# Kernel optimization log

Measured on AMD Instinct MI355X. Metric: run time of the kernel, lower is better.

## Reference

```python
import jax, jax.numpy as jnp
import numpy as np

N_NODES = 50000
N_EDGES = 800000
IN_DIM = 512
OUT_DIM = 512


def setup_inputs() -> dict:
    key = jax.random.key(0)
    ks = jax.random.split(key, 8)
    x = jax.random.normal(ks[0], (N_NODES, IN_DIM), dtype=jnp.float32)
    edge_index = jax.random.randint(ks[1], (2, N_EDGES), 0, N_NODES, dtype=jnp.int64)
    s = 1.0 / np.sqrt(IN_DIM)
    # SAGEConv params: lin_l (applied to aggregated neighbors, with bias),
    # lin_r (applied to root/self features, no bias). Two convs: loc and scale.
    Wl1 = jax.random.uniform(ks[2], (OUT_DIM, IN_DIM), jnp.float32, -s, s)
    bl1 = jnp.zeros((OUT_DIM,), jnp.float32)
    Wr1 = jax.random.uniform(ks[3], (OUT_DIM, IN_DIM), jnp.float32, -s, s)
    Wl2 = jax.random.uniform(ks[4], (OUT_DIM, IN_DIM), jnp.float32, -s, s)
    bl2 = jnp.zeros((OUT_DIM,), jnp.float32)
    Wr2 = jax.random.uniform(ks[5], (OUT_DIM, IN_DIM), jnp.float32, -s, s)
    return {"x": x, "edge_index": edge_index,
            "Wl1": Wl1, "bl1": bl1, "Wr1": Wr1,
            "Wl2": Wl2, "bl2": bl2, "Wr2": Wr2}


def _sage_conv(x, agg, Wl, bl, Wr):
    # lin_l(sum-aggregated neighbors) + lin_r(x)
    return agg @ Wl.T + bl + x @ Wr.T


def reference(x, edge_index, Wl1, bl1, Wr1, Wl2, bl2, Wr2):
    src, dst = edge_index[0], edge_index[1]
    # sum aggregation of source features into destination nodes: [N, in_dim]
    agg = jax.ops.segment_sum(x[src], dst, num_segments=N_NODES)
    loc = _sage_conv(x, agg, Wl1, bl1, Wr1)
    loc = jnp.clip(loc, -100.0, 100.0)
    scale = jax.nn.softplus(_sage_conv(x, agg, Wl2, bl2, Wr2)) + 0.001
    scale = jnp.minimum(scale, 100.0)
    return (loc, scale)
```

## Files before the change

### kernel.cpp

```cpp
#include <hip/hip_runtime.h>
#include <stdint.h>

#define N_NODES 50000
#define N_EDGES 800000
#define IN_DIM 512
#define OUT_DIM 512
#define KDIM 1024
#define NDIM 1024

typedef __bf16 bf16x8 __attribute__((ext_vector_type(8)));
typedef float f32x4 __attribute__((ext_vector_type(4)));

__device__ __forceinline__ unsigned short f2bf(float f) {
    union { float f; unsigned u; } c; c.f = f;
    unsigned u = c.u;
    u += 0x7fffu + ((u >> 16) & 1u);
    return (unsigned short)(u >> 16);
}
__device__ __forceinline__ float bf2f(unsigned short h) {
    union { unsigned u; float f; } c; c.u = ((unsigned)h) << 16;
    return c.f;
}

__global__ void xconv_kernel(const float* __restrict__ x, unsigned short* __restrict__ xb) {
    int i = blockIdx.x * blockDim.x + threadIdx.x;
    const int n4 = N_NODES * IN_DIM / 4;
    if (i < n4) {
        float4 v = ((const float4*)x)[i];
        ushort4 o;
        o.x = f2bf(v.x); o.y = f2bf(v.y); o.z = f2bf(v.z); o.w = f2bf(v.w);
        ((ushort4*)xb)[i] = o;
    }
}

__global__ void count_kernel(const int* __restrict__ ei, int* __restrict__ counts) {
    int i = blockIdx.x * blockDim.x + threadIdx.x;
    if (i < N_EDGES) {
        int dst = ei[N_EDGES + i];
        dst = min(max(dst, 0), N_NODES - 1);
        atomicAdd(&counts[dst], 1);
    }
}

__global__ __launch_bounds__(1024) void scan_local_kernel(
    const int* __restrict__ cnt, int* __restrict__ offs,
    int* __restrict__ bsums, int n) {
    __shared__ int warp_sums[16];
    int tid = threadIdx.x;
    int lane = tid & 63;
    int w = tid >> 6;
    int i = blockIdx.x * 1024 + tid;
    int v = (i < n) ? cnt[i] : 0;
    int s = v;
    #pragma unroll
    for (int d = 1; d < 64; d <<= 1) {
        int t = __shfl_up(s, d, 64);
        if (lane >= d) s += t;
    }
    if (lane == 63) warp_sums[w] = s;
    __syncthreads();
    if (w == 0) {
        int ws = (lane < 16) ? warp_sums[lane] : 0;
        #pragma unroll
        for (int d = 1; d < 16; d <<= 1) {
            int t = __shfl_up(ws, d, 64);
            if (lane >= d) ws += t;
        }
        if (lane < 16) warp_sums[lane] = ws;
    }
    __syncthreads();
    int base = (w > 0 ? warp_sums[w - 1] : 0);
    if (i < n) offs[i] = base + s - v;
    if (tid == 1023) bsums[blockIdx.x] = base + s;
}

__global__ void scan_bsums_kernel(int* __restrict__ bsums, int nb) {
    int lane = threadIdx.x & 63;
    int v = (lane < nb) ? bsums[lane] : 0;
    int s = v;
    #pragma unroll
    for (int d = 1; d < 64; d <<= 1) {
        int t = __shfl_up(s, d, 64);
        if (lane >= d) s += t;
    }
    if (lane < nb) bsums[lane] = s - v;
}

__global__ __launch_bounds__(1024) void scan_apply_kernel(
    int* __restrict__ offs, int* __restrict__ cursor,
    const int* __restrict__ bsums, const int* __restrict__ cnt, int n) {
    int i = blockIdx.x * 1024 + threadIdx.x;
    if (i < n) {
        int o = offs[i] + bsums[blockIdx.x];
        offs[i] = o;
        cursor[i] = o;
        if (i == n - 1) offs[n] = o + cnt[i];
    }
}

__global__ void fill_kernel(const int* __restrict__ ei, int* __restrict__ cursor,
                            int* __restrict__ bucket) {
    int i = blockIdx.x * blockDim.x + threadIdx.x;
    if (i < N_EDGES) {
        int src = ei[i];
        int dst = ei[N_EDGES + i];
        src = min(max(src, 0), N_NODES - 1);
        dst = min(max(dst, 0), N_NODES - 1);
        int pos = atomicAdd(&cursor[dst], 1);
        bucket[pos] = src;
    }
}

__global__ __launch_bounds__(256) void aggregate_kernel(
    const unsigned short* __restrict__ xb, const int* __restrict__ offs,
    const int* __restrict__ bucket, unsigned short* __restrict__ aggb) {
    int wid = threadIdx.x >> 6;
    int lane = threadIdx.x & 63;
    int n = blockIdx.x * 4 + wid;
    if (n >= N_NODES) return;
    int beg = offs[n], end = offs[n + 1];
    float a0[8] = {}, a1[8] = {};
    int e = beg;
    for (; e + 4 <= end; e += 4) {
        int s0 = bucket[e + 0];
        int s1 = bucket[e + 1];
        int s2 = bucket[e + 2];
        int s3 = bucket[e + 3];
        uint4 v0 = *(const uint4*)(xb + (size_t)s0 * IN_DIM + lane * 8);
        uint4 v1 = *(const uint4*)(xb + (size_t)s1 * IN_DIM + lane * 8);
        uint4 v2 = *(const uint4*)(xb + (size_t)s2 * IN_DIM + lane * 8);
        uint4 v3 = *(const uint4*)(xb + (size_t)s3 * IN_DIM + lane * 8);
        a0[0] += bf2f((unsigned short)(v0.x & 0xffffu)); a0[1] += bf2f((unsigned short)(v0.x >> 16));
        a0[2] += bf2f((unsigned short)(v0.y & 0xffffu)); a0[3] += bf2f((unsigned short)(v0.y >> 16));
        a0[4] += bf2f((unsigned short)(v0.z & 0xffffu)); a0[5] += bf2f((unsigned short)(v0.z >> 16));
        a0[6] += bf2f((unsigned short)(v0.w & 0xffffu)); a0[7] += bf2f((unsigned short)(v0.w >> 16));
        a1[0] += bf2f((unsigned short)(v1.x & 0xffffu)); a1[1] += bf2f((unsigned short)(v1.x >> 16));
        a1[2] += bf2f((unsigned short)(v1.y & 0xffffu)); a1[3] += bf2f((unsigned short)(v1.y >> 16));
        a1[4] += bf2f((unsigned short)(v1.z & 0xffffu)); a1[5] += bf2f((unsigned short)(v1.z >> 16));
        a1[6] += bf2f((unsigned short)(v1.w & 0xffffu)); a1[7] += bf2f((unsigned short)(v1.w >> 16));
        a0[0] += bf2f((unsigned short)(v2.x & 0xffffu)); a0[1] += bf2f((unsigned short)(v2.x >> 16));
        a0[2] += bf2f((unsigned short)(v2.y & 0xffffu)); a0[3] += bf2f((unsigned short)(v2.y >> 16));
        a0[4] += bf2f((unsigned short)(v2.z & 0xffffu)); a0[5] += bf2f((unsigned short)(v2.z >> 16));
        a0[6] += bf2f((unsigned short)(v2.w & 0xffffu)); a0[7] += bf2f((unsigned short)(v2.w >> 16));
        a1[0] += bf2f((unsigned short)(v3.x & 0xffffu)); a1[1] += bf2f((unsigned short)(v3.x >> 16));
        a1[2] += bf2f((unsigned short)(v3.y & 0xffffu)); a1[3] += bf2f((unsigned short)(v3.y >> 16));
        a1[4] += bf2f((unsigned short)(v3.z & 0xffffu)); a1[5] += bf2f((unsigned short)(v3.z >> 16));
        a1[6] += bf2f((unsigned short)(v3.w & 0xffffu)); a1[7] += bf2f((unsigned short)(v3.w >> 16));
    }
    for (; e < end; ++e) {
        int s = bucket[e];
        uint4 v = *(const uint4*)(xb + (size_t)s * IN_DIM + lane * 8);
        a0[0] += bf2f((unsigned short)(v.x & 0xffffu)); a0[1] += bf2f((unsigned short)(v.x >> 16));
        a0[2] += bf2f((unsigned short)(v.y & 0xffffu)); a0[3] += bf2f((unsigned short)(v.y >> 16));
        a0[4] += bf2f((unsigned short)(v.z & 0xffffu)); a0[5] += bf2f((unsigned short)(v.z >> 16));
        a0[6] += bf2f((unsigned short)(v.w & 0xffffu)); a0[7] += bf2f((unsigned short)(v.w >> 16));
    }
    uint4 o;
    o.x = (unsigned)f2bf(a0[0] + a1[0]) | ((unsigned)f2bf(a0[1] + a1[1]) << 16);
    o.y = (unsigned)f2bf(a0[2] + a1[2]) | ((unsigned)f2bf(a0[3] + a1[3]) << 16);
    o.z = (unsigned)f2bf(a0[4] + a1[4]) | ((unsigned)f2bf(a0[5] + a1[5]) << 16);
    o.w = (unsigned)f2bf(a0[6] + a1[6]) | ((unsigned)f2bf(a0[7] + a1[7]) << 16);
    *(uint4*)(aggb + (size_t)n * IN_DIM + lane * 8) = o;
}

__global__ void wconv_kernel(const float* __restrict__ Wl1, const float* __restrict__ Wr1,
                             const float* __restrict__ Wl2, const float* __restrict__ Wr2,
                             unsigned short* __restrict__ Wb) {
    int i = blockIdx.x * blockDim.x + threadIdx.x;
    if (i < NDIM * KDIM) {
        int n = i >> 10, k = i & 1023;
        const float* src;
        if (n < 512) src = (k < 512) ? Wl1 : Wr1;
        else         src = (k < 512) ? Wl2 : Wr2;
        int nn = n & 511, kk = k & 511;
        Wb[i] = f2bf(src[nn * 512 + kk]);
    }
}

#define BM 128
#define BN 128
#define BK 64
#define NT_TILES (NDIM / BN)
#define MT_TILES ((N_NODES + BM - 1) / BM)
#define NWG (NT_TILES * MT_TILES)

__device__ __forceinline__ void async_copy16(const void* g, void* lds) {
    __builtin_amdgcn_global_load_lds((const __attribute__((address_space(1))) void*)g,
                                     (__attribute__((address_space(3))) void*)lds, 16, 0, 0);
}

__global__ __launch_bounds__(256, 2) void gemm_kernel(
    const unsigned short* __restrict__ aggb,
    const unsigned short* __restrict__ xb,
    const unsigned short* __restrict__ Wb,
    const float* __restrict__ bl1, const float* __restrict__ bl2,
    float* __restrict__ out) {
    constexpr int M = N_NODES;
    __shared__ unsigned short sA[BM * BK];
    __shared__ unsigned short sB[BN * BK];

    int bid = blockIdx.x;
    int logical = (bid & 7) * (NWG / 8) + (bid >> 3);
    int nt = logical & (NT_TILES - 1);
    int mt = logical >> 3;
    int n0 = nt * BN;
    int m0 = mt * BM;

    int tid = threadIdx.x;
    int lane = tid & 63;
    int w = tid >> 6;
    int wm = (w >> 1) * 64, wn = (w & 1) * 64;

    f32x4 acc[4][4] = {};

    int fr = lane & 15, q = lane >> 4;
    int sl0 = ((q ^ (fr & 7)) << 3);
    int sl1 = (((q + 4) ^ (fr & 7)) << 3);

    for (int k0 = 0; k0 < KDIM; k0 += BK) {
        const unsigned short* Asrc;
        int ak;
        if (k0 < 512) { Asrc = aggb; ak = k0; } else { Asrc = xb; ak = k0 - 512; }
        #pragma unroll
        for (int iss = 0; iss < 4; ++iss) {
            int C = iss * 256 + tid;
            int r = C >> 3, p = C & 7;
            int gr = m0 + r; if (gr >= M) gr = M - 1;
            const unsigned short* g = Asrc + (size_t)gr * 512 + ak + ((p ^ (r & 7)) << 3);
            async_copy16(g, sA + (size_t)(iss * 256 + w * 64) * 8);
        }
        #pragma unroll
        for (int iss = 0; iss < 4; ++iss) {
            int C = iss * 256 + tid;
            int r = C >> 3, p = C & 7;
            const unsigned short* g = Wb + (size_t)(n0 + r) * KDIM + k0 + ((p ^ (r & 7)) << 3);
            async_copy16(g, sB + (size_t)(iss * 256 + w * 64) * 8);
        }
        __syncthreads();

        #pragma unroll
        for (int ksub = 0; ksub < 2; ++ksub) {
            int sl = ksub ? sl1 : sl0;
            bf16x8 af[4], bfg[4];
            #pragma unroll
            for (int i = 0; i < 4; ++i)
                af[i] = *(const bf16x8*)(sA + (wm + i * 16 + fr) * BK + sl);
            #pragma unroll
            for (int j = 0; j < 4; ++j)
                bfg[j] = *(const bf16x8*)(sB + (wn + j * 16 + fr) * BK + sl);
            #pragma unroll
            for (int i = 0; i < 4; ++i)
                #pragma unroll
                for (int j = 0; j < 4; ++j)
                    acc[i][j] = __builtin_amdgcn_mfma_f32_16x16x32_bf16(af[i], bfg[j], acc[i][j], 0, 0, 0);
        }
        __syncthreads();
    }

    bool is_scale = (n0 >= 512);
    const float* bias = is_scale ? bl2 : bl1;
    float* obase = out + (is_scale ? (size_t)N_NODES * OUT_DIM : 0);
    int ncol0 = is_scale ? (n0 - 512) : n0;
    int rq = lane >> 4;
    #pragma unroll
    for (int i = 0; i < 4; ++i) {
        #pragma unroll
        for (int j = 0; j < 4; ++j) {
            int colg = ncol0 + wn + j * 16 + fr;
            float b = bias[colg];
            #pragma unroll
            for (int r = 0; r < 4; ++r) {
                int rowg = m0 + wm + i * 16 + rq * 4 + r;
                if (rowg < M) {
                    float v = acc[i][j][r] + b;
                    float res;
                    if (is_scale) {
                        float sp = fmaxf(v, 0.f) + __logf(1.f + __expf(-fabsf(v)));
                        res = fminf(sp + 0.001f, 100.f);
                    } else {
                        res = fminf(fmaxf(v, -100.f), 100.f);
                    }
                    __builtin_nontemporal_store(res, &obase[(size_t)rowg * OUT_DIM + colg]);
                }
            }
        }
    }
}

extern "C" void kernel_launch(void* const* d_in, const int* in_sizes, int n_in,
                              void* d_out, int out_size, void* d_ws, size_t ws_size,
                              hipStream_t stream) {
    const float* x       = (const float*)d_in[0];
    const int* ei        = (const int*)d_in[1];
    const float* Wl1     = (const float*)d_in[2];
    const float* bl1     = (const float*)d_in[3];
    const float* Wr1     = (const float*)d_in[4];
    const float* Wl2     = (const float*)d_in[5];
    const float* bl2     = (const float*)d_in[6];
    const float* Wr2     = (const float*)d_in[7];
    float* out = (float*)d_out;

    char* ws = (char*)d_ws;
    size_t off = 0;
    auto alloc = [&](size_t bytes) -> void* {
        void* p = ws + off;
        off = (off + bytes + 255) & ~(size_t)255;
        return p;
    };
    unsigned short* xb    = (unsigned short*)alloc((size_t)N_NODES * IN_DIM * 2);
    unsigned short* aggb  = (unsigned short*)alloc((size_t)N_NODES * IN_DIM * 2);
    unsigned short* Wb    = (unsigned short*)alloc((size_t)NDIM * KDIM * 2);
    int* counts           = (int*)alloc((size_t)(N_NODES + 1) * 4);
    int* offs             = (int*)alloc((size_t)(N_NODES + 1) * 4);
    int* cursor           = (int*)alloc((size_t)N_NODES * 4);
    int* bucket           = (int*)alloc((size_t)N_EDGES * 4);
    int* bsums            = (int*)alloc(64 * 4);

    hipMemsetAsync(counts, 0, (size_t)(N_NODES + 1) * 4, stream);

    const int nb = (N_NODES + 1023) / 1024;

    xconv_kernel<<<(N_NODES * IN_DIM / 4 + 255) / 256, 256, 0, stream>>>(x, xb);
    count_kernel<<<(N_EDGES + 255) / 256, 256, 0, stream>>>(ei, counts);
    scan_local_kernel<<<nb, 1024, 0, stream>>>(counts, offs, bsums, N_NODES);
    scan_bsums_kernel<<<1, 64, 0, stream>>>(bsums, nb);
    scan_apply_kernel<<<nb, 1024, 0, stream>>>(offs, cursor, bsums, counts, N_NODES);
    fill_kernel<<<(N_EDGES + 255) / 256, 256, 0, stream>>>(ei, cursor, bucket);
    aggregate_kernel<<<(N_NODES + 3) / 4, 256, 0, stream>>>(xb, offs, bucket, aggb);
    wconv_kernel<<<(NDIM * KDIM + 255) / 256, 256, 0, stream>>>(Wl1, Wr1, Wl2, Wr2, Wb);

    gemm_kernel<<<NWG, 256, 0, stream>>>(aggb, xb, Wb, bl1, bl2, out);
}
```

Baseline: 600.0 us.

## Fuse prep kernels, merge scan steps, unroll gather, double-buffer GEMM LDS

```diff
diff --git a/kernel.cpp b/kernel.cpp
--- a/kernel.cpp
+++ b/kernel.cpp
@@ -22,23 +22,43 @@
     return c.f;
 }
 
-__global__ void xconv_kernel(const float* __restrict__ x, unsigned short* __restrict__ xb) {
-    int i = blockIdx.x * blockDim.x + threadIdx.x;
-    const int n4 = N_NODES * IN_DIM / 4;
-    if (i < n4) {
-        float4 v = ((const float4*)x)[i];
-        ushort4 o;
-        o.x = f2bf(v.x); o.y = f2bf(v.y); o.z = f2bf(v.z); o.w = f2bf(v.w);
-        ((ushort4*)xb)[i] = o;
-    }
-}
-
-__global__ void count_kernel(const int* __restrict__ ei, int* __restrict__ counts) {
-    int i = blockIdx.x * blockDim.x + threadIdx.x;
-    if (i < N_EDGES) {
-        int dst = ei[N_EDGES + i];
-        dst = min(max(dst, 0), N_NODES - 1);
-        atomicAdd(&counts[dst], 1);
+#define XCONV_BLOCKS ((N_NODES * IN_DIM / 4 + 255) / 256)
+#define COUNT_BLOCKS ((N_EDGES + 255) / 256)
+#define WCONV_BLOCKS ((NDIM * KDIM + 255) / 256)
+
+__global__ __launch_bounds__(256) void prep_kernel(
+    const float* __restrict__ x, unsigned short* __restrict__ xb,
+    const int* __restrict__ ei, int* __restrict__ counts,
+    const float* __restrict__ Wl1, const float* __restrict__ Wr1,
+    const float* __restrict__ Wl2, const float* __restrict__ Wr2,
+    unsigned short* __restrict__ Wb) {
+    int b = blockIdx.x;
+    if (b < XCONV_BLOCKS) {
+        int i = b * 256 + threadIdx.x;
+        const int n4 = N_NODES * IN_DIM / 4;
+        if (i < n4) {
+            float4 v = ((const float4*)x)[i];
+            ushort4 o;
+            o.x = f2bf(v.x); o.y = f2bf(v.y); o.z = f2bf(v.z); o.w = f2bf(v.w);
+            ((ushort4*)xb)[i] = o;
+        }
+    } else if (b < XCONV_BLOCKS + COUNT_BLOCKS) {
+        int i = (b - XCONV_BLOCKS) * 256 + threadIdx.x;
+        if (i < N_EDGES) {
+            int dst = ei[N_EDGES + i];
+            dst = min(max(dst, 0), N_NODES - 1);
+            atomicAdd(&counts[dst], 1);
+        }
+    } else {
+        int i = (b - XCONV_BLOCKS - COUNT_BLOCKS) * 256 + threadIdx.x;
+        if (i < NDIM * KDIM) {
+            int n = i >> 10, k = i & 1023;
+            const float* src;
+            if (n < 512) src = (k < 512) ? Wl1 : Wr1;
+            else         src = (k < 512) ? Wl2 : Wr2;
+            int nn = n & 511, kk = k & 511;
+            Wb[i] = f2bf(src[nn * 512 + kk]);
+        }
     }
 }
 
@@ -74,24 +94,21 @@
     if (tid == 1023) bsums[blockIdx.x] = base + s;
 }
 
-__global__ void scan_bsums_kernel(int* __restrict__ bsums, int nb) {
-    int lane = threadIdx.x & 63;
-    int v = (lane < nb) ? bsums[lane] : 0;
-    int s = v;
-    #pragma unroll
-    for (int d = 1; d < 64; d <<= 1) {
-        int t = __shfl_up(s, d, 64);
-        if (lane >= d) s += t;
-    }
-    if (lane < nb) bsums[lane] = s - v;
-}
-
 __global__ __launch_bounds__(1024) void scan_apply_kernel(
     int* __restrict__ offs, int* __restrict__ cursor,
     const int* __restrict__ bsums, const int* __restrict__ cnt, int n) {
-    int i = blockIdx.x * 1024 + threadIdx.x;
+    __shared__ int s_base;
+    int tid = threadIdx.x;
+    if (tid < 64) {
+        int v = (tid < (int)blockIdx.x) ? bsums[tid] : 0;
+        #pragma unroll
+        for (int d = 32; d > 0; d >>= 1) v += __shfl_down(v, d, 64);
+        if (tid == 0) s_base = v;
+    }
+    __syncthreads();
+    int i = blockIdx.x * 1024 + tid;
     if (i < n) {
-        int o = offs[i] + bsums[blockIdx.x];
+        int o = offs[i] + s_base;
         offs[i] = o;
         cursor[i] = o;
         if (i == n - 1) offs[n] = o + cnt[i];
@@ -121,31 +138,21 @@
     int beg = offs[n], end = offs[n + 1];
     float a0[8] = {}, a1[8] = {};
     int e = beg;
-    for (; e + 4 <= end; e += 4) {
-        int s0 = bucket[e + 0];
-        int s1 = bucket[e + 1];
-        int s2 = bucket[e + 2];
-        int s3 = bucket[e + 3];
-        uint4 v0 = *(const uint4*)(xb + (size_t)s0 * IN_DIM + lane * 8);
-        uint4 v1 = *(const uint4*)(xb + (size_t)s1 * IN_DIM + lane * 8);
-        uint4 v2 = *(const uint4*)(xb + (size_t)s2 * IN_DIM + lane * 8);
-        uint4 v3 = *(const uint4*)(xb + (size_t)s3 * IN_DIM + lane * 8);
-        a0[0] += bf2f((unsigned short)(v0.x & 0xffffu)); a0[1] += bf2f((unsigned short)(v0.x >> 16));
-        a0[2] += bf2f((unsigned short)(v0.y & 0xffffu)); a0[3] += bf2f((unsigned short)(v0.y >> 16));
-        a0[4] += bf2f((unsigned short)(v0.z & 0xffffu)); a0[5] += bf2f((unsigned short)(v0.z >> 16));
-        a0[6] += bf2f((unsigned short)(v0.w & 0xffffu)); a0[7] += bf2f((unsigned short)(v0.w >> 16));
-        a1[0] += bf2f((unsigned short)(v1.x & 0xffffu)); a1[1] += bf2f((unsigned short)(v1.x >> 16));
-        a1[2] += bf2f((unsigned short)(v1.y & 0xffffu)); a1[3] += bf2f((unsigned short)(v1.y >> 16));
-        a1[4] += bf2f((unsigned short)(v1.z & 0xffffu)); a1[5] += bf2f((unsigned short)(v1.z >> 16));
-        a1[6] += bf2f((unsigned short)(v1.w & 0xffffu)); a1[7] += bf2f((unsigned short)(v1.w >> 16));
-        a0[0] += bf2f((unsigned short)(v2.x & 0xffffu)); a0[1] += bf2f((unsigned short)(v2.x >> 16));
-        a0[2] += bf2f((unsigned short)(v2.y & 0xffffu)); a0[3] += bf2f((unsigned short)(v2.y >> 16));
-        a0[4] += bf2f((unsigned short)(v2.z & 0xffffu)); a0[5] += bf2f((unsigned short)(v2.z >> 16));
-        a0[6] += bf2f((unsigned short)(v2.w & 0xffffu)); a0[7] += bf2f((unsigned short)(v2.w >> 16));
-        a1[0] += bf2f((unsigned short)(v3.x & 0xffffu)); a1[1] += bf2f((unsigned short)(v3.x >> 16));
-        a1[2] += bf2f((unsigned short)(v3.y & 0xffffu)); a1[3] += bf2f((unsigned short)(v3.y >> 16));
-        a1[4] += bf2f((unsigned short)(v3.z & 0xffffu)); a1[5] += bf2f((unsigned short)(v3.z >> 16));
-        a1[6] += bf2f((unsigned short)(v3.w & 0xffffu)); a1[7] += bf2f((unsigned short)(v3.w >> 16));
+    for (; e + 8 <= end; e += 8) {
+        int idx[8];
+        #pragma unroll
+        for (int u = 0; u < 8; ++u) idx[u] = bucket[e + u];
+        uint4 v[8];
+        #pragma unroll
+        for (int u = 0; u < 8; ++u) v[u] = *(const uint4*)(xb + (size_t)idx[u] * IN_DIM + lane * 8);
+        #pragma unroll
+        for (int u = 0; u < 8; ++u) {
+            float* a = (u & 1) ? a1 : a0;
+            a[0] += bf2f((unsigned short)(v[u].x & 0xffffu)); a[1] += bf2f((unsigned short)(v[u].x >> 16));
+            a[2] += bf2f((unsigned short)(v[u].y & 0xffffu)); a[3] += bf2f((unsigned short)(v[u].y >> 16));
+            a[4] += bf2f((unsigned short)(v[u].z & 0xffffu)); a[5] += bf2f((unsigned short)(v[u].z >> 16));
+            a[6] += bf2f((unsigned short)(v[u].w & 0xffffu)); a[7] += bf2f((unsigned short)(v[u].w >> 16));
+        }
     }
     for (; e < end; ++e) {
         int s = bucket[e];
@@ -163,26 +170,13 @@
     *(uint4*)(aggb + (size_t)n * IN_DIM + lane * 8) = o;
 }
 
-__global__ void wconv_kernel(const float* __restrict__ Wl1, const float* __restrict__ Wr1,
-                             const float* __restrict__ Wl2, const float* __restrict__ Wr2,
-                             unsigned short* __restrict__ Wb) {
-    int i = blockIdx.x * blockDim.x + threadIdx.x;
-    if (i < NDIM * KDIM) {
-        int n = i >> 10, k = i & 1023;
-        const float* src;
-        if (n < 512) src = (k < 512) ? Wl1 : Wr1;
-        else         src = (k < 512) ? Wl2 : Wr2;
-        int nn = n & 511, kk = k & 511;
-        Wb[i] = f2bf(src[nn * 512 + kk]);
-    }
-}
-
 #define BM 128
 #define BN 128
 #define BK 64
 #define NT_TILES (NDIM / BN)
 #define MT_TILES ((N_NODES + BM - 1) / BM)
 #define NWG (NT_TILES * MT_TILES)
+#define NKT (KDIM / BK)
 
 __device__ __forceinline__ void async_copy16(const void* g, void* lds) {
     __builtin_amdgcn_global_load_lds((const __attribute__((address_space(1))) void*)g,
@@ -196,8 +190,8 @@
     const float* __restrict__ bl1, const float* __restrict__ bl2,
     float* __restrict__ out) {
     constexpr int M = N_NODES;
-    __shared__ unsigned short sA[BM * BK];
-    __shared__ unsigned short sB[BN * BK];
+    __shared__ unsigned short sA[2][BM * BK];
+    __shared__ unsigned short sB[2][BN * BK];
 
     int bid = blockIdx.x;
     int logical = (bid & 7) * (NWG / 8) + (bid >> 3);
@@ -217,43 +211,54 @@
     int sl0 = ((q ^ (fr & 7)) << 3);
     int sl1 = (((q + 4) ^ (fr & 7)) << 3);
 
-    for (int k0 = 0; k0 < KDIM; k0 += BK) {
-        const unsigned short* Asrc;
-        int ak;
-        if (k0 < 512) { Asrc = aggb; ak = k0; } else { Asrc = xb; ak = k0 - 512; }
+    auto STAGE = [&](int t, int buf) {
+        if (t >= NKT) return;
+        int kk = t * BK;
+        const unsigned short* Asrc = (kk < 512) ? aggb : xb;
+        int ak = kk & 511;
         #pragma unroll
         for (int iss = 0; iss < 4; ++iss) {
             int C = iss * 256 + tid;
             int r = C >> 3, p = C & 7;
             int gr = m0 + r; if (gr >= M) gr = M - 1;
             const unsigned short* g = Asrc + (size_t)gr * 512 + ak + ((p ^ (r & 7)) << 3);
-            async_copy16(g, sA + (size_t)(iss * 256 + w * 64) * 8);
+            async_copy16(g, &sA[buf][(size_t)(iss * 256 + (tid & ~63)) * 8]);
         }
         #pragma unroll
         for (int iss = 0; iss < 4; ++iss) {
             int C = iss * 256 + tid;
             int r = C >> 3, p = C & 7;
-            const unsigned short* g = Wb + (size_t)(n0 + r) * KDIM + k0 + ((p ^ (r & 7)) << 3);
-            async_copy16(g, sB + (size_t)(iss * 256 + w * 64) * 8);
-        }
-        __syncthreads();
-
+            const unsigned short* g = Wb + (size_t)(n0 + r) * KDIM + kk + ((p ^ (r & 7)) << 3);
+            async_copy16(g, &sB[buf][(size_t)(iss * 256 + (tid & ~63)) * 8]);
+        }
+    };
+    auto COMPUTE = [&](int buf) {
         #pragma unroll
         for (int ksub = 0; ksub < 2; ++ksub) {
             int sl = ksub ? sl1 : sl0;
             bf16x8 af[4], bfg[4];
             #pragma unroll
             for (int i = 0; i < 4; ++i)
-                af[i] = *(const bf16x8*)(sA + (wm + i * 16 + fr) * BK + sl);
+                af[i] = *(const bf16x8*)(&sA[buf][0] + (wm + i * 16 + fr) * BK + sl);
             #pragma unroll
             for (int j = 0; j < 4; ++j)
-                bfg[j] = *(const bf16x8*)(sB + (wn + j * 16 + fr) * BK + sl);
+                bfg[j] = *(const bf16x8*)(&sB[buf][0] + (wn + j * 16 + fr) * BK + sl);
             #pragma unroll
             for (int i = 0; i < 4; ++i)
                 #pragma unroll
                 for (int j = 0; j < 4; ++j)
                     acc[i][j] = __builtin_amdgcn_mfma_f32_16x16x32_bf16(af[i], bfg[j], acc[i][j], 0, 0, 0);
         }
+    };
+
+    STAGE(0, 0);
+    __syncthreads();
+    for (int t = 0; t < NKT; t += 2) {
+        STAGE(t + 1, 1);
+        COMPUTE(0);
+        __syncthreads();
+        STAGE(t + 2, 0);
+        COMPUTE(1);
         __syncthreads();
     }
 
@@ -320,14 +325,12 @@
 
     const int nb = (N_NODES + 1023) / 1024;
 
-    xconv_kernel<<<(N_NODES * IN_DIM / 4 + 255) / 256, 256, 0, stream>>>(x, xb);
-    count_kernel<<<(N_EDGES + 255) / 256, 256, 0, stream>>>(ei, counts);
+    prep_kernel<<<XCONV_BLOCKS + COUNT_BLOCKS + WCONV_BLOCKS, 256, 0, stream>>>(
+        x, xb, ei, counts, Wl1, Wr1, Wl2, Wr2, Wb);
     scan_local_kernel<<<nb, 1024, 0, stream>>>(counts, offs, bsums, N_NODES);
-    scan_bsums_kernel<<<1, 64, 0, stream>>>(bsums, nb);
     scan_apply_kernel<<<nb, 1024, 0, stream>>>(offs, cursor, bsums, counts, N_NODES);
     fill_kernel<<<(N_EDGES + 255) / 256, 256, 0, stream>>>(ei, cursor, bucket);
     aggregate_kernel<<<(N_NODES + 3) / 4, 256, 0, stream>>>(xb, offs, bucket, aggb);
-    wconv_kernel<<<(NDIM * KDIM + 255) / 256, 256, 0, stream>>>(Wl1, Wr1, Wl2, Wr2, Wb);
 
     gemm_kernel<<<NWG, 256, 0, stream>>>(aggb, xb, Wb, bl1, bl2, out);
 }
```

After: 622.8 us. +3.8%, slower.
